# Kernel optimization log

Hardware: AMD Instinct MI355X
Metric: run time of the kernel (lower is better)

## Reference

```python
import jax, jax.numpy as jnp
import numpy as np

K_HARRIS = 0.04
RATIO = 0.5

# Sobel kernels exactly as in the torch module, shape (1,3,3,3) = (O_dummy, kd, kh, kw)
_sx2d = np.array([[-1.0, 0.0, 1.0], [-2.0, 0.0, 2.0], [-1.0, 0.0, 1.0]], dtype=np.float32)
_SOBEL_X = np.broadcast_to(_sx2d, (3, 3, 3)).copy()[None]            # same 3x3 plane at each depth
_SOBEL_Y = np.broadcast_to(_sx2d.T, (3, 3, 3)).copy()[None]          # [[-1,-2,-1],[0,0,0],[1,2,1]] planes
_SOBEL_Z = np.stack([-np.ones((3, 3), np.float32),
                     np.zeros((3, 3), np.float32),
                     np.ones((3, 3), np.float32)])[None]


def _dwconv3d(x, w):
    """Depthwise 3x3x3 conv, padding=1. x: [B,C,D,H,W], w: [C,1,3,3,3]."""
    return jax.lax.conv_general_dilated(
        x, w,
        window_strides=(1, 1, 1),
        padding=((1, 1), (1, 1), (1, 1)),
        dimension_numbers=("NCDHW", "OIDHW", "NCDHW"),
        feature_group_count=x.shape[1])


def setup_inputs() -> dict:
    key = jax.random.key(0)
    x = jax.random.normal(key, (1, 16, 64, 96, 96), dtype=jnp.float32)
    return {
        "x": x,
        "weight_x": jnp.asarray(_SOBEL_X),
        "weight_y": jnp.asarray(_SOBEL_Y),
        "weight_z": jnp.asarray(_SOBEL_Z),
    }


def reference(x, weight_x, weight_y, weight_z):
    B, C, D, H, W = x.shape
    # expand (1,3,3,3) params to depthwise kernels (C,1,3,3,3)
    wx = jnp.broadcast_to(weight_x[None], (C, 1, 3, 3, 3))
    wy = jnp.broadcast_to(weight_y[None], (C, 1, 3, 3, 3))
    wz = jnp.broadcast_to(weight_z[None], (C, 1, 3, 3, 3))

    gx = _dwconv3d(x, wx)
    gy = _dwconv3d(x, wy)
    gz = _dwconv3d(x, wz)

    # 3x3x3 box filter (mean) applied to structure-tensor entries
    box = jnp.ones((C, 1, 3, 3, 3), dtype=x.dtype) / 27.0
    gx2 = _dwconv3d(gx * gx, box)
    gy2 = _dwconv3d(gy * gy, box)
    gz2 = _dwconv3d(gz * gz, box)
    gxy = _dwconv3d(gx * gy, box)
    gxz = _dwconv3d(gx * gz, box)
    gyz = _dwconv3d(gy * gz, box)

    det = (gx2 * (gy2 * gz2 - gyz * gyz)
           - gxy * (gxy * gz2 - gyz * gxz)
           + gxz * (gxy * gyz - gy2 * gxz))
    trace = gx2 + gy2 + gz2
    harris = det - K_HARRIS * trace * trace

    p = jnp.sum(harris, axis=(-1, -2, -3))          # [B, C]
    k = int(RATIO * C)
    _, idx = jax.lax.top_k(p, k)                     # [B, k]
    # gather selected channels: [B, k, D, H, W]
    return jnp.take_along_axis(x, idx[:, :, None, None, None], axis=1)
```

## Files before the change

### kernel.cpp

```cpp
#include <hip/hip_runtime.h>

#define CCH 16
#define DD 64
#define HH 96
#define WW 96
#define HW (HH*WW)
#define DHW (DD*HH*WW)
#define CH4 (DHW/4)
#define NTH 768
#define DCH 16
#define NBY (DD/DCH)
#define KTR 1.08f
#define INV27C (1.f/19683.f)

typedef float v2f __attribute__((ext_vector_type(2)));

__device__ __forceinline__ float dpp_up(float v) {
    return __int_as_float(__builtin_amdgcn_update_dpp(
        0, __float_as_int(v), 0x111 , 0xF, 0xF, true));
}
__device__ __forceinline__ float dpp_dn(float v) {
    return __int_as_float(__builtin_amdgcn_update_dpp(
        0, __float_as_int(v), 0x101 , 0xF, 0xF, true));
}

__global__ __launch_bounds__(NTH, 6)
void harris_sum_kernel(const float* __restrict__ x, float* __restrict__ pp) {
    __shared__ float red[12];

    const int tid = threadIdx.x;
    const int lh = tid & 15, lc = tid >> 4;
    const int c  = blockIdx.z;
    const int H0 = blockIdx.x * 12;
    const int o0 = blockIdx.y * DCH;
    const int gh = H0 + lh - 2;
    const bool rowok = ((unsigned)gh < HH);
    const float mask = rowok ? 1.f : 0.f;
    const bool lok = (lc > 0), rok = (lc < 47);
    const float maskl = lok ? mask : 0.f;
    const float maskr = rok ? mask : 0.f;
    const float* xc = x + (size_t)c * DHW;
    const int woff = gh * WW + (lc << 1);

    v2f Lp,Cp,Rp, Lm,Cm,Rm, Ln,Cn,Rn, Lf,Cf,Rf;

    auto loadslice = [&](int e, v2f& L, v2f& C, v2f& R) {
        if (rowok && (unsigned)e < DD) {
            const float* s = xc + (size_t)e * HW + woff;
            const float2 t = *(const float2*)s;
            C.x = t.x; C.y = t.y;
            if (lok) { const float2 u = *(const float2*)(s - 2); L.x = u.x; L.y = u.y; }
            else     { L.x = 0.f; L.y = 0.f; }
            if (rok) { const float2 u = *(const float2*)(s + 2); R.x = u.x; R.y = u.y; }
            else     { R.x = 0.f; R.y = 0.f; }
        } else {
            L.x=0.f; L.y=0.f; C.x=0.f; C.y=0.f; R.x=0.f; R.y=0.f;
        }
    };

    loadslice(o0 - 2, Lp, Cp, Rp);
    loadslice(o0 - 1, Lm, Cm, Rm);
    loadslice(o0,     Ln, Cn, Rn);

    v2f s2m1[6], s2m2[6];
    #pragma unroll
    for (int f = 0; f < 6; ++f) {
        s2m1[f].x = 0.f; s2m1[f].y = 0.f;
        s2m2[f].x = 0.f; s2m2[f].y = 0.f;
    }
    v2f hv; hv.x = 0.f; hv.y = 0.f;
    const bool emit_row = (lh >= 2) && (lh <= 13);

    #pragma unroll
    for (int k = 0; k < DCH + 2; ++k) {
        const int e = o0 - 1 + k;
        if (k <= DCH) loadslice(e + 2, Lf, Cf, Rf);
        else { Lf.x=0.f;Lf.y=0.f; Cf.x=0.f;Cf.y=0.f; Rf.x=0.f;Rf.y=0.f; }

        v2f s2c[6];
        if ((unsigned)e < DD) {
            const v2f AL = (Lp + Lm) + Ln;
            const v2f AC = (Cp + Cm) + Cn;
            const v2f AR = (Rp + Rm) + Rn;
            const v2f DL = Ln - Lp;
            const v2f DC = Cn - Cp;
            const v2f DR = Rn - Rp;

            const float Sxl = AC.x - AL.x, Sx0 = AC.y - AL.y,
                        Sx1 = AR.x - AC.x, Sxr = AR.y - AC.y;
            const float Txl = AL.x + 2.f*AL.y + AC.x, Tx0 = AL.y + 2.f*AC.x + AC.y,
                        Tx1 = AC.x + 2.f*AC.y + AR.x, Txr = AC.y + 2.f*AR.x + AR.y;
            const float Tdl = DL.x + DL.y + DC.x, Td0 = DL.y + DC.x + DC.y,
                        Td1 = DC.x + DC.y + DR.x, Tdr = DC.y + DR.x + DR.y;

            const float glx = (dpp_up(Sxl) + 2.f*Sxl + dpp_dn(Sxl)) * maskl;
            const float gly = (dpp_dn(Txl) - dpp_up(Txl)) * maskl;
            const float glz = (dpp_up(Tdl) + Tdl + dpp_dn(Tdl)) * maskl;
            const float gx0 = (dpp_up(Sx0) + 2.f*Sx0 + dpp_dn(Sx0)) * mask;
            const float gy0 = (dpp_dn(Tx0) - dpp_up(Tx0)) * mask;
            const float gz0 = (dpp_up(Td0) + Td0 + dpp_dn(Td0)) * mask;
            const float gx1 = (dpp_up(Sx1) + 2.f*Sx1 + dpp_dn(Sx1)) * mask;
            const float gy1 = (dpp_dn(Tx1) - dpp_up(Tx1)) * mask;
            const float gz1 = (dpp_up(Td1) + Td1 + dpp_dn(Td1)) * mask;
            const float grx = (dpp_up(Sxr) + 2.f*Sxr + dpp_dn(Sxr)) * maskr;
            const float gry = (dpp_dn(Txr) - dpp_up(Txr)) * maskr;
            const float grz = (dpp_up(Tdr) + Tdr + dpp_dn(Tdr)) * maskr;

            v2f gxv, gyv, gzv;
            gxv.x = gx0; gxv.y = gx1; gyv.x = gy0; gyv.y = gy1; gzv.x = gz0; gzv.y = gz1;
            const v2f Pxx = gxv*gxv, Pyy = gyv*gyv, Pzz = gzv*gzv;
            const v2f Pxy = gxv*gyv, Pxz = gxv*gzv, Pyz = gyv*gzv;
            const float Plxx = glx*glx, Plyy = gly*gly, Plzz = glz*glz;
            const float Plxy = glx*gly, Plxz = glx*glz, Plyz = gly*glz;
            const float Prxx = grx*grx, Pryy = gry*gry, Przz = grz*grz;
            const float Prxy = grx*gry, Prxz = grx*grz, Pryz = gry*grz;

            #define FIELD(f, Pv, Pl, Pr)                                   \
            {   const float s_ = (Pv).x + (Pv).y;                          \
                const float R0 = (Pl) + s_, R1 = s_ + (Pr);                \
                s2c[f].x = dpp_up(R0) + R0 + dpp_dn(R0);                   \
                s2c[f].y = dpp_up(R1) + R1 + dpp_dn(R1); }
            FIELD(0, Pxx, Plxx, Prxx)
            FIELD(1, Pyy, Plyy, Pryy)
            FIELD(2, Pzz, Plzz, Przz)
            FIELD(3, Pxy, Plxy, Prxy)
            FIELD(4, Pxz, Plxz, Prxz)
            FIELD(5, Pyz, Plyz, Pryz)
            #undef FIELD
        } else {
            #pragma unroll
            for (int f = 0; f < 6; ++f) { s2c[f].x = 0.f; s2c[f].y = 0.f; }
        }

        if (k >= 2 && emit_row) {
            const v2f sxx = s2m2[0] + s2m1[0] + s2c[0];
            const v2f syy = s2m2[1] + s2m1[1] + s2c[1];
            const v2f szz = s2m2[2] + s2m1[2] + s2c[2];
            const v2f sxy = s2m2[3] + s2m1[3] + s2c[3];
            const v2f sxz = s2m2[4] + s2m1[4] + s2c[4];
            const v2f syz = s2m2[5] + s2m1[5] + s2c[5];
            const v2f det = sxx*(syy*szz - syz*syz)
                          - sxy*(sxy*szz - syz*sxz)
                          + sxz*(sxy*syz - syy*sxz);
            const v2f tr = sxx + syy + szz;
            hv += det - KTR * (tr * tr);
        }
        #pragma unroll
        for (int f = 0; f < 6; ++f) { s2m2[f] = s2m1[f]; s2m1[f] = s2c[f]; }
        Lp = Lm; Cp = Cm; Rp = Rm;
        Lm = Ln; Cm = Cn; Rm = Rn;
        Ln = Lf; Cn = Cf; Rn = Rf;
    }

    float hs = hv.x + hv.y;
    #pragma unroll
    for (int o = 32; o > 0; o >>= 1) hs += __shfl_down(hs, o, 64);
    if ((tid & 63) == 0) red[tid >> 6] = hs;
    __syncthreads();
    if (tid == 0) {
        float s = 0.f;
        #pragma unroll
        for (int i = 0; i < 12; ++i) s += red[i];
        pp[c * 32 + blockIdx.y * 8 + blockIdx.x] = s * INV27C;
    }
}

__global__ __launch_bounds__(256)
void gather_topk_kernel(const float* __restrict__ x, const float* __restrict__ pp,
                        float4* __restrict__ out) {
    __shared__ float pv[CCH];
    __shared__ int sidx[8];
    const int tid = threadIdx.x;
    if (tid < CCH) {
        float s = 0.f;
        #pragma unroll
        for (int j = 0; j < 32; ++j) s += pp[tid * 32 + j];
        pv[tid] = s;
    }
    __syncthreads();
    if (tid < CCH) {
        const float v = pv[tid];
        int r = 0;
        #pragma unroll
        for (int i = 0; i < CCH; ++i) {
            const float u = pv[i];
            r += (u > v) || (u == v && i < tid);
        }
        if (r < 8) sidx[r] = tid;
    }
    __syncthreads();
    const int j   = blockIdx.y;
    const int pos = blockIdx.x * 256 + tid;
    const int cidx = sidx[j];
    const float4* src = (const float4*)(x + (size_t)cidx * DHW);
    out[(size_t)j * CH4 + pos] = src[pos];
}

extern "C" void kernel_launch(void* const* d_in, const int* in_sizes, int n_in,
                              void* d_out, int out_size, void* d_ws, size_t ws_size,
                              hipStream_t stream) {
    const float* x = (const float*)d_in[0];
    float4* out = reinterpret_cast<float4*>(d_out);
    float* pp = (float*)d_ws;

    dim3 g1(8, NBY, CCH);
    harris_sum_kernel<<<g1, NTH, 0, stream>>>(x, pp);

    dim3 g2(CH4 / 256, 8, 1);
    gather_topk_kernel<<<g2, 256, 0, stream>>>(x, pp, out);
}
```

Before: 136.6 us.

## Branchless clamped loads in Harris kernel and split top-k from gather

The Harris kernel now clamps row and depth indices and always issues its loads, zeroing out-of-range values with mask multiplies instead of branches. The slice loop is partially unrolled by 3 rather than fully unrolled, the emit-row test becomes a multiply, and some arithmetic is reassociated into FMAs. The top-k selection moves into its own single-block kernel, so each gather block no longer re-sums the 512 partials and re-ranks the channels. Gather blocks now copy four float4 values each. The trade is an extra kernel launch, plus clamped loads that always fetch memory even for rows and slices that get discarded.

```diff
diff --git a/kernel.cpp b/kernel.cpp
--- a/kernel.cpp
+++ b/kernel.cpp
@@ -35,27 +35,34 @@
     const int o0 = blockIdx.y * DCH;
     const int gh = H0 + lh - 2;
     const bool rowok = ((unsigned)gh < HH);
-    const float mask = rowok ? 1.f : 0.f;
     const bool lok = (lc > 0), rok = (lc < 47);
-    const float maskl = lok ? mask : 0.f;
-    const float maskr = rok ? mask : 0.f;
+    const float mask  = rowok ? 1.f : 0.f;
+    const float maskl = (rowok && lok) ? 1.f : 0.f;
+    const float maskr = (rowok && rok) ? 1.f : 0.f;
+    const v2f mcv = {mask,  mask};
+    const v2f mlv = {maskl, maskl};
+    const v2f mrv = {maskr, maskr};
+    const float em = (lh >= 2 && lh <= 13) ? 1.f : 0.f;
+    const v2f emv = {em, em};
+
+    const int ghc   = min(max(gh, 0), HH - 1);
+    const int woffc = ghc * WW + (lc << 1);
+    const int woffl = lok ? woffc - 2 : woffc;
+    const int woffr = rok ? woffc + 2 : woffc;
     const float* xc = x + (size_t)c * DHW;
-    const int woff = gh * WW + (lc << 1);
-
-    v2f Lp,Cp,Rp, Lm,Cm,Rm, Ln,Cn,Rn, Lf,Cf,Rf;
+
+    v2f Lp,Cp,Rp, Lm,Cm,Rm, Ln,Cn,Rn;
 
     auto loadslice = [&](int e, v2f& L, v2f& C, v2f& R) {
-        if (rowok && (unsigned)e < DD) {
-            const float* s = xc + (size_t)e * HW + woff;
-            const float2 t = *(const float2*)s;
-            C.x = t.x; C.y = t.y;
-            if (lok) { const float2 u = *(const float2*)(s - 2); L.x = u.x; L.y = u.y; }
-            else     { L.x = 0.f; L.y = 0.f; }
-            if (rok) { const float2 u = *(const float2*)(s + 2); R.x = u.x; R.y = u.y; }
-            else     { R.x = 0.f; R.y = 0.f; }
-        } else {
-            L.x=0.f; L.y=0.f; C.x=0.f; C.y=0.f; R.x=0.f; R.y=0.f;
+        const int ec = min(max(e, 0), DD - 1);
+        const float* sp = xc + (size_t)(ec * HW);
+        C = *(const v2f*)(sp + woffc);
+        L = *(const v2f*)(sp + woffl);
+        R = *(const v2f*)(sp + woffr);
+        if (e != ec) {
+            L = (v2f){0.f,0.f}; C = (v2f){0.f,0.f}; R = (v2f){0.f,0.f};
         }
+        L *= mlv; C *= mcv; R *= mrv;
     };
 
     loadslice(o0 - 2, Lp, Cp, Rp);
@@ -65,85 +72,83 @@
     v2f s2m1[6], s2m2[6];
     #pragma unroll
     for (int f = 0; f < 6; ++f) {
-        s2m1[f].x = 0.f; s2m1[f].y = 0.f;
-        s2m2[f].x = 0.f; s2m2[f].y = 0.f;
-    }
-    v2f hv; hv.x = 0.f; hv.y = 0.f;
-    const bool emit_row = (lh >= 2) && (lh <= 13);
-
-    #pragma unroll
+        s2m1[f] = (v2f){0.f,0.f};
+        s2m2[f] = (v2f){0.f,0.f};
+    }
+    v2f hv = {0.f, 0.f};
+
+    #pragma unroll 3
     for (int k = 0; k < DCH + 2; ++k) {
         const int e = o0 - 1 + k;
-        if (k <= DCH) loadslice(e + 2, Lf, Cf, Rf);
-        else { Lf.x=0.f;Lf.y=0.f; Cf.x=0.f;Cf.y=0.f; Rf.x=0.f;Rf.y=0.f; }
+        v2f Lf = {0.f,0.f}, Cf = {0.f,0.f}, Rf = {0.f,0.f};
+        if (k < DCH + 1) loadslice(e + 2, Lf, Cf, Rf);
+
+        const v2f AL = (Lp + Lm) + Ln;
+        const v2f AC = (Cp + Cm) + Cn;
+        const v2f AR = (Rp + Rm) + Rn;
+        const v2f DL = Ln - Lp;
+        const v2f DC = Cn - Cp;
+        const v2f DR = Rn - Rp;
+
+        const v2f SxA = AC - AL;
+        const v2f SxB = AR - AC;
+        const float Txl = fmaf(2.f, AL.y, AL.x + AC.x);
+        const float Tx0 = fmaf(2.f, AC.x, AL.y + AC.y);
+        const float Tx1 = fmaf(2.f, AC.y, AC.x + AR.x);
+        const float Txr = fmaf(2.f, AR.x, AC.y + AR.y);
+        const float p01 = DL.y + DC.x, p23 = DC.y + DR.x;
+        const float Tdl = DL.x + p01,  Td0 = p01 + DC.y;
+        const float Td1 = DC.x + p23,  Tdr = p23 + DR.y;
+
+        #define HX(S)  ((dpp_up(S) + (S)) + (dpp_dn(S) + (S)))
+        #define HY(T)  (dpp_dn(T) - dpp_up(T))
+        #define HZ(T)  ((dpp_up(T) + (T)) + dpp_dn(T))
+        const float glx = HX(SxA.x) * maskl;
+        const float gx0 = HX(SxA.y) * mask;
+        const float gx1 = HX(SxB.x) * mask;
+        const float grx = HX(SxB.y) * maskr;
+        const float gly = HY(Txl) * maskl;
+        const float gy0 = HY(Tx0) * mask;
+        const float gy1 = HY(Tx1) * mask;
+        const float gry = HY(Txr) * maskr;
+        const float glz = HZ(Tdl) * maskl;
+        const float gz0 = HZ(Td0) * mask;
+        const float gz1 = HZ(Td1) * mask;
+        const float grz = HZ(Tdr) * maskr;
+        #undef HX
+        #undef HY
+        #undef HZ
+
+        const v2f gxv = {gx0, gx1}, gyv = {gy0, gy1}, gzv = {gz0, gz1};
+        const v2f Pxx = gxv*gxv, Pyy = gyv*gyv, Pzz = gzv*gzv;
+        const v2f Pxy = gxv*gyv, Pxz = gxv*gzv, Pyz = gyv*gzv;
 
         v2f s2c[6];
-        if ((unsigned)e < DD) {
-            const v2f AL = (Lp + Lm) + Ln;
-            const v2f AC = (Cp + Cm) + Cn;
-            const v2f AR = (Rp + Rm) + Rn;
-            const v2f DL = Ln - Lp;
-            const v2f DC = Cn - Cp;
-            const v2f DR = Rn - Rp;
-
-            const float Sxl = AC.x - AL.x, Sx0 = AC.y - AL.y,
-                        Sx1 = AR.x - AC.x, Sxr = AR.y - AC.y;
-            const float Txl = AL.x + 2.f*AL.y + AC.x, Tx0 = AL.y + 2.f*AC.x + AC.y,
-                        Tx1 = AC.x + 2.f*AC.y + AR.x, Txr = AC.y + 2.f*AR.x + AR.y;
-            const float Tdl = DL.x + DL.y + DC.x, Td0 = DL.y + DC.x + DC.y,
-                        Td1 = DC.x + DC.y + DR.x, Tdr = DC.y + DR.x + DR.y;
-
-            const float glx = (dpp_up(Sxl) + 2.f*Sxl + dpp_dn(Sxl)) * maskl;
-            const float gly = (dpp_dn(Txl) - dpp_up(Txl)) * maskl;
-            const float glz = (dpp_up(Tdl) + Tdl + dpp_dn(Tdl)) * maskl;
-            const float gx0 = (dpp_up(Sx0) + 2.f*Sx0 + dpp_dn(Sx0)) * mask;
-            const float gy0 = (dpp_dn(Tx0) - dpp_up(Tx0)) * mask;
-            const float gz0 = (dpp_up(Td0) + Td0 + dpp_dn(Td0)) * mask;
-            const float gx1 = (dpp_up(Sx1) + 2.f*Sx1 + dpp_dn(Sx1)) * mask;
-            const float gy1 = (dpp_dn(Tx1) - dpp_up(Tx1)) * mask;
-            const float gz1 = (dpp_up(Td1) + Td1 + dpp_dn(Td1)) * mask;
-            const float grx = (dpp_up(Sxr) + 2.f*Sxr + dpp_dn(Sxr)) * maskr;
-            const float gry = (dpp_dn(Txr) - dpp_up(Txr)) * maskr;
-            const float grz = (dpp_up(Tdr) + Tdr + dpp_dn(Tdr)) * maskr;
-
-            v2f gxv, gyv, gzv;
-            gxv.x = gx0; gxv.y = gx1; gyv.x = gy0; gyv.y = gy1; gzv.x = gz0; gzv.y = gz1;
-            const v2f Pxx = gxv*gxv, Pyy = gyv*gyv, Pzz = gzv*gzv;
-            const v2f Pxy = gxv*gyv, Pxz = gxv*gzv, Pyz = gyv*gzv;
-            const float Plxx = glx*glx, Plyy = gly*gly, Plzz = glz*glz;
-            const float Plxy = glx*gly, Plxz = glx*glz, Plyz = gly*glz;
-            const float Prxx = grx*grx, Pryy = gry*gry, Przz = grz*grz;
-            const float Prxy = grx*gry, Prxz = grx*grz, Pryz = gry*grz;
-
-            #define FIELD(f, Pv, Pl, Pr)                                   \
-            {   const float s_ = (Pv).x + (Pv).y;                          \
-                const float R0 = (Pl) + s_, R1 = s_ + (Pr);                \
-                s2c[f].x = dpp_up(R0) + R0 + dpp_dn(R0);                   \
-                s2c[f].y = dpp_up(R1) + R1 + dpp_dn(R1); }
-            FIELD(0, Pxx, Plxx, Prxx)
-            FIELD(1, Pyy, Plyy, Pryy)
-            FIELD(2, Pzz, Plzz, Przz)
-            FIELD(3, Pxy, Plxy, Prxy)
-            FIELD(4, Pxz, Plxz, Prxz)
-            FIELD(5, Pyz, Plyz, Pryz)
-            #undef FIELD
-        } else {
-            #pragma unroll
-            for (int f = 0; f < 6; ++f) { s2c[f].x = 0.f; s2c[f].y = 0.f; }
-        }
-
-        if (k >= 2 && emit_row) {
-            const v2f sxx = s2m2[0] + s2m1[0] + s2c[0];
-            const v2f syy = s2m2[1] + s2m1[1] + s2c[1];
-            const v2f szz = s2m2[2] + s2m1[2] + s2c[2];
-            const v2f sxy = s2m2[3] + s2m1[3] + s2c[3];
-            const v2f sxz = s2m2[4] + s2m1[4] + s2c[4];
-            const v2f syz = s2m2[5] + s2m1[5] + s2c[5];
+        #define FIELD(f, Pv, Pl, Pr)                                   \
+        {   const float s_ = (Pv).x + (Pv).y;                          \
+            const float R0 = (Pl) + s_, R1 = s_ + (Pr);                \
+            s2c[f].x = (dpp_up(R0) + R0) + dpp_dn(R0);                 \
+            s2c[f].y = (dpp_up(R1) + R1) + dpp_dn(R1); }
+        FIELD(0, Pxx, glx*glx, grx*grx)
+        FIELD(1, Pyy, gly*gly, gry*gry)
+        FIELD(2, Pzz, glz*glz, grz*grz)
+        FIELD(3, Pxy, glx*gly, grx*gry)
+        FIELD(4, Pxz, glx*glz, grx*grz)
+        FIELD(5, Pyz, gly*glz, gry*grz)
+        #undef FIELD
+
+        if (k >= 2) {
+            const v2f sxx = (s2m2[0] + s2m1[0]) + s2c[0];
+            const v2f syy = (s2m2[1] + s2m1[1]) + s2c[1];
+            const v2f szz = (s2m2[2] + s2m1[2]) + s2c[2];
+            const v2f sxy = (s2m2[3] + s2m1[3]) + s2c[3];
+            const v2f sxz = (s2m2[4] + s2m1[4]) + s2c[4];
+            const v2f syz = (s2m2[5] + s2m1[5]) + s2c[5];
             const v2f det = sxx*(syy*szz - syz*syz)
                           - sxy*(sxy*szz - syz*sxz)
                           + sxz*(sxy*syz - syy*sxz);
-            const v2f tr = sxx + syy + szz;
-            hv += det - KTR * (tr * tr);
+            const v2f tr = (sxx + syy) + szz;
+            hv += (det - KTR*(tr*tr)) * emv;
         }
         #pragma unroll
         for (int f = 0; f < 6; ++f) { s2m2[f] = s2m1[f]; s2m1[f] = s2c[f]; }
@@ -165,35 +170,40 @@
     }
 }
 
-__global__ __launch_bounds__(256)
-void gather_topk_kernel(const float* __restrict__ x, const float* __restrict__ pp,
-                        float4* __restrict__ out) {
+__global__ __launch_bounds__(64)
+void topk_select_kernel(const float* __restrict__ pp, int* __restrict__ sidx) {
     __shared__ float pv[CCH];
-    __shared__ int sidx[8];
-    const int tid = threadIdx.x;
-    if (tid < CCH) {
+    const int t = threadIdx.x;
+    if (t < CCH) {
         float s = 0.f;
         #pragma unroll
-        for (int j = 0; j < 32; ++j) s += pp[tid * 32 + j];
-        pv[tid] = s;
+        for (int j = 0; j < 32; ++j) s += pp[t * 32 + j];
+        pv[t] = s;
     }
     __syncthreads();
-    if (tid < CCH) {
-        const float v = pv[tid];
+    if (t < CCH) {
+        const float v = pv[t];
         int r = 0;
         #pragma unroll
         for (int i = 0; i < CCH; ++i) {
             const float u = pv[i];
-            r += (u > v) || (u == v && i < tid);
+            r += (u > v) || (u == v && i < t);
         }
-        if (r < 8) sidx[r] = tid;
-    }
-    __syncthreads();
-    const int j   = blockIdx.y;
-    const int pos = blockIdx.x * 256 + tid;
+        if (r < 8) sidx[r] = t;
+    }
+}
+
+__global__ __launch_bounds__(256)
+void gather_kernel(const float* __restrict__ x, const int* __restrict__ sidx,
+                   float4* __restrict__ out) {
+    const int j = blockIdx.y;
     const int cidx = sidx[j];
     const float4* src = (const float4*)(x + (size_t)cidx * DHW);
-    out[(size_t)j * CH4 + pos] = src[pos];
+    float4* dst = out + (size_t)j * CH4;
+    const int base = blockIdx.x * 1024 + threadIdx.x;
+    #pragma unroll
+    for (int t = 0; t < 4; ++t)
+        dst[base + t * 256] = src[base + t * 256];
 }
 
 extern "C" void kernel_launch(void* const* d_in, const int* in_sizes, int n_in,
@@ -202,10 +212,13 @@
     const float* x = (const float*)d_in[0];
     float4* out = reinterpret_cast<float4*>(d_out);
     float* pp = (float*)d_ws;
+    int* sidx = (int*)(pp + 512);
 
     dim3 g1(8, NBY, CCH);
     harris_sum_kernel<<<g1, NTH, 0, stream>>>(x, pp);
 
-    dim3 g2(CH4 / 256, 8, 1);
-    gather_topk_kernel<<<g2, 256, 0, stream>>>(x, pp, out);
-}
+    topk_select_kernel<<<1, 64, 0, stream>>>(pp, sidx);
+
+    dim3 g3(CH4 / 1024, 8, 1);
+    gather_kernel<<<g3, 256, 0, stream>>>(x, sidx, out);
+}
```

After: 182.8 us. 33.8% more time.
